# Performance work log

Hardware: AMD Instinct MI355X
Metric: run time of the kernel (lower is better)

The kernel has to match this reference:

```python
import jax, jax.numpy as jnp
import numpy as np

NUM_HEADS = 16  # matches init_kwargs num_heads
ROPE_BASE = 10000.0


def _rope(x):
    # x: [B, H, T, d_k]; canonical interleaved rotary embedding
    d = x.shape[-1]
    T = x.shape[-2]
    inv_freq = 1.0 / (ROPE_BASE ** (jnp.arange(0, d, 2, dtype=jnp.float32) / d))  # [d/2]
    ang = jnp.arange(T, dtype=jnp.float32)[:, None] * inv_freq[None, :]  # [T, d/2]
    cos, sin = jnp.cos(ang), jnp.sin(ang)  # broadcast over B,H
    x1 = x[..., 0::2]
    x2 = x[..., 1::2]
    even = x1 * cos - x2 * sin
    odd = x1 * sin + x2 * cos
    return jnp.stack([even, odd], axis=-1).reshape(x.shape)


def setup_inputs() -> dict:
    key = jax.random.key(0)
    ks = jax.random.split(key, 5)
    B, T, D = 2, 2048, 2048
    s = 1.0 / np.sqrt(D)
    return {
        "x": jax.random.normal(ks[0], (B, T, D), dtype=jnp.float32),
        "Wkqv": jax.random.normal(ks[1], (D, 3 * D), dtype=jnp.float32) * s,
        "bkqv": jax.random.normal(ks[2], (3 * D,), dtype=jnp.float32) * 0.01,
        "Wo": jax.random.normal(ks[3], (D, D), dtype=jnp.float32) * s,
        "bo": jax.random.normal(ks[4], (D,), dtype=jnp.float32) * 0.01,
    }


def reference(x, Wkqv, bkqv, Wo, bo):
    B, T, D = x.shape
    H = NUM_HEADS
    d_k = D // H
    kqv = x @ Wkqv + bkqv  # [B, T, 3D]
    # split order per source: index 0 = K, 1 = Q, 2 = V
    k, q, v = jnp.split(kqv, 3, axis=-1)

    def heads(t):  # [B, T, D] -> [B, H, T, d_k]
        return t.reshape(B, T, H, d_k).transpose(0, 2, 1, 3)

    k, q, v = heads(k), heads(q), heads(v)
    k = _rope(k)
    q = _rope(q)
    scores = jnp.einsum('bhtd,bhTd->bhtT', q, k)  # [B, H, T, T]
    causal = jnp.triu(jnp.ones((T, T), dtype=bool), k=1)
    scores = jnp.where(causal, -jnp.inf, scores)
    attn = jax.nn.softmax(scores / jnp.sqrt(jnp.float32(d_k)), axis=-1)
    out = jnp.einsum('bhtT,bhTd->bhtd', attn, v)  # [B, H, T, d_k]
    out = out.transpose(0, 2, 1, 3).reshape(B, T, D)
    return out @ Wo + bo
```

## Files before the change

### kernel.cpp

```cpp
#include <hip/hip_runtime.h>
#include <cstdint>
#include <cstddef>

typedef __attribute__((ext_vector_type(4))) float  floatx4;
typedef __attribute__((ext_vector_type(8))) __bf16 bf16x8;
typedef __attribute__((ext_vector_type(4))) __bf16 bf16x4;

#define B_   2
#define T_   2048
#define D_   2048
#define H_   16
#define DK   128
#define BT_  (B_ * T_)
#define N3   (3 * D_)

__device__ __forceinline__ void async_copy16(const void* g, void* l) {
    __builtin_amdgcn_global_load_lds((const __attribute__((address_space(1))) void*)g,
                                     (__attribute__((address_space(3))) void*)l,
                                     16, 0, 0);
}

__global__ void cast_bf16_kernel(const float* __restrict__ in, __bf16* __restrict__ out, int n4) {
    int i = blockIdx.x * 256 + threadIdx.x;
    if (i >= n4) return;
    float4 v = ((const float4*)in)[i];
    bf16x4 o;
    o.x = (__bf16)v.x; o.y = (__bf16)v.y; o.z = (__bf16)v.z; o.w = (__bf16)v.w;
    ((bf16x4*)out)[i] = o;
}

__global__ __launch_bounds__(256)
void transcast_kernel(const float* __restrict__ in, __bf16* __restrict__ out, int R, int C) {
    __shared__ float tile[64][65];
    const int tid = threadIdx.x;
    const int r0 = blockIdx.y * 64, c0 = blockIdx.x * 64;
#pragma unroll
    for (int p = 0; p < 4; ++p) {
        int u = p * 256 + tid;
        int r = u >> 4, c4 = (u & 15) * 4;
        float4 v = *(const float4*)(in + (size_t)(r0 + r) * C + c0 + c4);
        tile[r][c4 + 0] = v.x; tile[r][c4 + 1] = v.y;
        tile[r][c4 + 2] = v.z; tile[r][c4 + 3] = v.w;
    }
    __syncthreads();
#pragma unroll
    for (int p = 0; p < 2; ++p) {
        int v = p * 256 + tid;
        int cc = v >> 3, rr = (v & 7) * 8;
        bf16x8 o;
#pragma unroll
        for (int i2 = 0; i2 < 8; ++i2) o[i2] = (__bf16)tile[rr + i2][cc];
        *(bf16x8*)(out + (size_t)(c0 + cc) * R + r0 + rr) = o;
    }
}

template <typename OutT>
__global__ __launch_bounds__(256)
void gemm_bt(const __bf16* __restrict__ A, const __bf16* __restrict__ BTm,
             const float* __restrict__ bias, OutT* __restrict__ C,
             int M, int N, int K) {
    __shared__ __align__(16) __bf16 As[128 * 64];
    __shared__ __align__(16) __bf16 Bs[128 * 64];
    const int tid  = threadIdx.x;
    const int lane = tid & 63;
    const int wave = tid >> 6;
    const int quad = lane >> 4;
    const int l16  = lane & 15;
    const int m0 = blockIdx.y * 128;
    const int n0 = blockIdx.x * 128;
    const int wm = (wave & 1) * 64;
    const int wn = (wave >> 1) * 64;

    const floatx4 z4 = {0.f, 0.f, 0.f, 0.f};
    floatx4 acc[4][4];
#pragma unroll
    for (int i = 0; i < 4; ++i)
#pragma unroll
        for (int j = 0; j < 4; ++j) acc[i][j] = z4;

    int           sOff[4];
    const __bf16* gA[4];
    const __bf16* gB[4];
#pragma unroll
    for (int i = 0; i < 4; ++i) {
        int s = i * 256 + tid;
        int row = s >> 3, cs = s & 7;
        int gc = cs ^ (row & 7);
        sOff[i] = s * 8;
        gA[i] = A   + (size_t)(m0 + row) * K + gc * 8;
        gB[i] = BTm + (size_t)(n0 + row) * K + gc * 8;
    }

    for (int kt = 0; kt < K; kt += 64) {
        __syncthreads();
#pragma unroll
        for (int i = 0; i < 4; ++i) {
            async_copy16(gA[i] + kt, As + sOff[i]);
            async_copy16(gB[i] + kt, Bs + sOff[i]);
        }
        __syncthreads();
#pragma unroll
        for (int ks2 = 0; ks2 < 2; ++ks2) {
            bf16x8 af[4], bf[4];
#pragma unroll
            for (int t = 0; t < 4; ++t) {
                int rowA = wm + t * 16 + l16;
                int ca = (ks2 * 4 + quad) ^ (rowA & 7);
                af[t] = *(const bf16x8*)(As + rowA * 64 + ca * 8);
                int rowB = wn + t * 16 + l16;
                int cb = (ks2 * 4 + quad) ^ (rowB & 7);
                bf[t] = *(const bf16x8*)(Bs + rowB * 64 + cb * 8);
            }
#pragma unroll
            for (int mt = 0; mt < 4; ++mt)
#pragma unroll
                for (int nt = 0; nt < 4; ++nt)
                    acc[mt][nt] = __builtin_amdgcn_mfma_f32_16x16x32_bf16(af[mt], bf[nt], acc[mt][nt], 0, 0, 0);
        }
    }

#pragma unroll
    for (int nt = 0; nt < 4; ++nt) {
        int n = n0 + wn + nt * 16 + l16;
        float bv = bias[n];
#pragma unroll
        for (int mt = 0; mt < 4; ++mt)
#pragma unroll
            for (int r = 0; r < 4; ++r) {
                int m = m0 + wm + mt * 16 + quad * 4 + r;
                C[(size_t)m * N + n] = (OutT)(acc[mt][nt][r] + bv);
            }
    }
}

__global__ __launch_bounds__(256)
void gemm_kqv(const __bf16* __restrict__ A, const __bf16* __restrict__ BTm,
              const float* __restrict__ bias,
              __bf16* __restrict__ Kh, __bf16* __restrict__ Qh,
              __bf16* __restrict__ VT,
              int M, int N, int K) {
    __shared__ __align__(16) __bf16 smem[128 * 136];
    __bf16* As = smem;
    __bf16* Bs = smem + 128 * 64;
    const int tid  = threadIdx.x;
    const int lane = tid & 63;
    const int wave = tid >> 6;
    const int quad = lane >> 4;
    const int l16  = lane & 15;
    const int m0 = blockIdx.y * 128;
    const int n0 = blockIdx.x * 128;
    const int wm = (wave & 1) * 64;
    const int wn = (wave >> 1) * 64;

    const floatx4 z4 = {0.f, 0.f, 0.f, 0.f};
    floatx4 acc[4][4];
#pragma unroll
    for (int i = 0; i < 4; ++i)
#pragma unroll
        for (int j = 0; j < 4; ++j) acc[i][j] = z4;

    int           sOff[4];
    const __bf16* gA[4];
    const __bf16* gB[4];
#pragma unroll
    for (int i = 0; i < 4; ++i) {
        int s = i * 256 + tid;
        int row = s >> 3, cs = s & 7;
        int gc = cs ^ (row & 7);
        sOff[i] = s * 8;
        gA[i] = A   + (size_t)(m0 + row) * K + gc * 8;
        gB[i] = BTm + (size_t)(n0 + row) * K + gc * 8;
    }

    for (int kt = 0; kt < K; kt += 64) {
        __syncthreads();
#pragma unroll
        for (int i = 0; i < 4; ++i) {
            async_copy16(gA[i] + kt, As + sOff[i]);
            async_copy16(gB[i] + kt, Bs + sOff[i]);
        }
        __syncthreads();
#pragma unroll
        for (int ks2 = 0; ks2 < 2; ++ks2) {
            bf16x8 af[4], bf[4];
#pragma unroll
            for (int t = 0; t < 4; ++t) {
                int rowA = wm + t * 16 + l16;
                int ca = (ks2 * 4 + quad) ^ (rowA & 7);
                af[t] = *(const bf16x8*)(As + rowA * 64 + ca * 8);
                int rowB = wn + t * 16 + l16;
                int cb = (ks2 * 4 + quad) ^ (rowB & 7);
                bf[t] = *(const bf16x8*)(Bs + rowB * 64 + cb * 8);
            }
#pragma unroll
            for (int mt = 0; mt < 4; ++mt)
#pragma unroll
                for (int nt = 0; nt < 4; ++nt)
                    acc[mt][nt] = __builtin_amdgcn_mfma_f32_16x16x32_bf16(af[mt], bf[nt], acc[mt][nt], 0, 0, 0);
        }
    }

    const int which = n0 >> 11;
    const int h  = (n0 & (D_ - 1)) >> 7;
    const int b  = m0 >> 11;
    const int t0 = m0 & (T_ - 1);
    const int bh = b * H_ + h;

    if (which == 2) {
        __syncthreads();
#pragma unroll
        for (int nt = 0; nt < 4; ++nt) {
            const int n  = n0 + wn + nt * 16 + l16;
            const float bv = bias[n];
            const int dd = wn + nt * 16 + l16;
#pragma unroll
            for (int mt = 0; mt < 4; ++mt)
#pragma unroll
                for (int r = 0; r < 4; ++r) {
                    const int tl = wm + mt * 16 + quad * 4 + r;
                    smem[dd * 136 + tl] = (__bf16)(acc[mt][nt][r] + bv);
                }
        }
        __syncthreads();
#pragma unroll
        for (int i = 0; i < 8; ++i) {
            int s = i * 256 + tid;
            int dd = s >> 4, c = s & 15;
            bf16x8 vv = *(const bf16x8*)(smem + dd * 136 + c * 8);
            *(bf16x8*)(VT + ((size_t)bh * DK + dd) * T_ + t0 + c * 8) = vv;
        }
    } else {
        const float qscale = which ? 0.12751740f : 1.0f;
        __bf16* dst = which ? Qh : Kh;
#pragma unroll
        for (int nt = 0; nt < 4; ++nt) {
            const int n  = n0 + wn + nt * 16 + l16;
            const float bv = bias[n];
            const int dd = wn + nt * 16 + l16;
            const float freq_rev = 0.15915494309189535f *
                exp2f((float)(dd >> 1) * (-13.287712379549449f / 64.f));
#pragma unroll
            for (int mt = 0; mt < 4; ++mt)
#pragma unroll
                for (int r = 0; r < 4; ++r) {
                    const int t = t0 + wm + mt * 16 + quad * 4 + r;
                    const float val = acc[mt][nt][r] + bv;
                    const float other = __shfl_xor(val, 1);
                    const float x1 = (dd & 1) ? other : val;
                    const float x2 = (dd & 1) ? val : other;
                    float rev = (float)t * freq_rev;
                    rev -= floorf(rev);
                    const float ang = rev * 6.283185307179586f;
                    const float sn = __sinf(ang), cn = __cosf(ang);
                    const float res = (dd & 1) ? (x1 * sn + x2 * cn)
                                               : (x1 * cn - x2 * sn);
                    dst[((size_t)bh * T_ + t) * DK + dd] = (__bf16)(res * qscale);
                }
        }
    }
}

__global__ __launch_bounds__(512)
void fa_kernel(const __bf16* __restrict__ Qg, const __bf16* __restrict__ Kg,
               const __bf16* __restrict__ VTg, __bf16* __restrict__ Og) {
    __shared__ __align__(16) __bf16 Ks[2][64 * 128];
    __shared__ __align__(16) __bf16 Vs[2][128 * 64];
    __shared__ __align__(16) __bf16 Ps[8][16 * 64];
    const int tid  = threadIdx.x;
    const int lane = tid & 63, wave = tid >> 6;
    const int quad = lane >> 4, l16 = lane & 15;
    const int bh = blockIdx.y;
    const int j  = blockIdx.x;
    const int b = bh >> 4, h = bh & 15;

    const __bf16* Kb = Kg  + (size_t)bh * T_ * DK;
    const __bf16* Vb = VTg + (size_t)bh * DK * T_;
    __bf16* Psw = Ps[wave];
    const int swzP = (l16 & 7) << 1;

    const floatx4 z4 = {0.f, 0.f, 0.f, 0.f};

    int           sK[2], sV[2];
    const __bf16* gK[2];
    const __bf16* gV[2];
#pragma unroll
    for (int i = 0; i < 2; ++i) {
        int s = i * 512 + tid;
        { int row = s >> 4, cs = s & 15; int gc = cs ^ (row & 7);
          sK[i] = s * 8; gK[i] = Kb + (size_t)row * DK + gc * 8; }
        { int row = s >> 3, cs = s & 7;  int gc = cs ^ (row & 7);
          sV[i] = s * 8; gV[i] = Vb + (size_t)row * T_ + gc * 8; }
    }

    for (int half = 0; half < 2; ++half) {
        const int qt = half ? (15 - j) : j;
        const int q0 = qt * 128;
        const int qpos = q0 + wave * 16 + l16;
        const int nkt = 2 * qt + 2;

        __syncthreads();
        {
            const __bf16* Qb = Qg + (size_t)(bh * T_ + q0) * DK;
#pragma unroll
            for (int i = 0; i < 4; ++i) {
                int s = i * 512 + tid;
                int row = s >> 4, cs = s & 15;
                int gc = cs ^ (row & 7);
                async_copy16(Qb + row * DK + gc * 8, &Ks[0][0] + s * 8);
            }
        }
        __syncthreads();
        bf16x8 qf[4];
#pragma unroll
        for (int ks = 0; ks < 4; ++ks) {
            int row = wave * 16 + l16;
            int c = (ks * 4 + quad) ^ (row & 7);
            qf[ks] = *(const bf16x8*)(&Ks[0][0] + row * DK + c * 8);
        }
        __syncthreads();

#pragma unroll
        for (int i = 0; i < 2; ++i) async_copy16(gK[i], &Ks[0][0] + sK[i]);
#pragma unroll
        for (int i = 0; i < 2; ++i) async_copy16(gV[i], &Vs[0][0] + sV[i]);

        float m_i = -1e30f, l_i = 0.f;
        floatx4 accO[8];
#pragma unroll
        for (int dt = 0; dt < 8; ++dt) accO[dt] = z4;

        for (int kt = 0; kt < nkt; ++kt) {
            const int cur = kt & 1;
            if (kt < nkt - 1) {
                const int nb = cur ^ 1;
                const size_t koff = (size_t)(kt + 1) * 64 * DK;
                const size_t voff = (size_t)(kt + 1) * 64;
#pragma unroll
                for (int i = 0; i < 2; ++i) async_copy16(gK[i] + koff, &Ks[nb][0] + sK[i]);
#pragma unroll
                for (int i = 0; i < 2; ++i) async_copy16(gV[i] + voff, &Vs[nb][0] + sV[i]);
                asm volatile("s_waitcnt vmcnt(4)" ::: "memory");
            } else {
                asm volatile("s_waitcnt vmcnt(0)" ::: "memory");
            }
            __builtin_amdgcn_s_barrier();

            const __bf16* Kcur = &Ks[cur][0];
            const __bf16* Vcur = &Vs[cur][0];

            floatx4 sc[4];
#pragma unroll
            for (int nt = 0; nt < 4; ++nt) sc[nt] = z4;
            __builtin_amdgcn_s_setprio(1);
#pragma unroll
            for (int ks = 0; ks < 4; ++ks)
#pragma unroll
                for (int nt = 0; nt < 4; ++nt) {
                    int row = nt * 16 + l16;
                    int c = (ks * 4 + quad) ^ (row & 7);
                    bf16x8 kf = *(const bf16x8*)(Kcur + row * DK + c * 8);
                    sc[nt] = __builtin_amdgcn_mfma_f32_16x16x32_bf16(kf, qf[ks], sc[nt], 0, 0, 0);
                }
            __builtin_amdgcn_s_setprio(0);

            float mnew = -1e30f;
            if (kt >= 2 * qt) {
#pragma unroll
                for (int nt = 0; nt < 4; ++nt) {
                    int kbase = kt * 64 + nt * 16 + quad * 4;
#pragma unroll
                    for (int r = 0; r < 4; ++r) {
                        float v = sc[nt][r];
                        v = (kbase + r > qpos) ? -1e30f : v;
                        sc[nt][r] = v;
                        mnew = fmaxf(mnew, v);
                    }
                }
            } else {
#pragma unroll
                for (int nt = 0; nt < 4; ++nt)
#pragma unroll
                    for (int r = 0; r < 4; ++r) mnew = fmaxf(mnew, sc[nt][r]);
            }
            mnew = fmaxf(mnew, __shfl_xor(mnew, 16));
            mnew = fmaxf(mnew, __shfl_xor(mnew, 32));
            const float mi = fmaxf(m_i, mnew);
            const float alpha = exp2f(m_i - mi);
            m_i = mi;

            float rs = 0.f;
#pragma unroll
            for (int nt = 0; nt < 4; ++nt)
#pragma unroll
                for (int r = 0; r < 4; ++r) {
                    float pv = exp2f(sc[nt][r] - mi);
                    sc[nt][r] = pv;
                    rs += pv;
                }
            rs += __shfl_xor(rs, 16);
            rs += __shfl_xor(rs, 32);
            l_i = l_i * alpha + rs;
#pragma unroll
            for (int dt = 0; dt < 8; ++dt)
#pragma unroll
                for (int r = 0; r < 4; ++r) accO[dt][r] *= alpha;

#pragma unroll
            for (int nt = 0; nt < 4; ++nt) {
                bf16x4 pw;
                pw.x = (__bf16)sc[nt][0]; pw.y = (__bf16)sc[nt][1];
                pw.z = (__bf16)sc[nt][2]; pw.w = (__bf16)sc[nt][3];
                int g = (nt * 4 + quad) ^ swzP;
                *(bf16x4*)(Psw + l16 * 64 + g * 4) = pw;
            }
            __builtin_amdgcn_s_setprio(1);
#pragma unroll
            for (int kc = 0; kc < 2; ++kc) {
                int gk = (kc * 8 + quad * 2) ^ swzP;
                bf16x8 pb = *(const bf16x8*)(Psw + l16 * 64 + gk * 4);
#pragma unroll
                for (int dt = 0; dt < 8; ++dt) {
                    int vrow = dt * 16 + l16;
                    int vch = (kc * 4 + quad) ^ (vrow & 7);
                    bf16x8 vf = *(const bf16x8*)(Vcur + vrow * 64 + vch * 8);
                    accO[dt] = __builtin_amdgcn_mfma_f32_16x16x32_bf16(vf, pb, accO[dt], 0, 0, 0);
                }
            }
            __builtin_amdgcn_s_setprio(0);

            __builtin_amdgcn_s_barrier();
        }

        const float inv = 1.0f / l_i;
        __bf16* orow = Og + (size_t)(b * T_ + qpos) * D_ + h * DK;
#pragma unroll
        for (int dt = 0; dt < 8; ++dt) {
            bf16x4 ow;
            ow.x = (__bf16)(accO[dt][0] * inv);
            ow.y = (__bf16)(accO[dt][1] * inv);
            ow.z = (__bf16)(accO[dt][2] * inv);
            ow.w = (__bf16)(accO[dt][3] * inv);
            *(bf16x4*)(orow + dt * 16 + quad * 4) = ow;
        }
    }
}

extern "C" void kernel_launch(void* const* d_in, const int* in_sizes, int n_in,
                              void* d_out, int out_size, void* d_ws, size_t ws_size,
                              hipStream_t stream) {
    const float* x    = (const float*)d_in[0];
    const float* Wkqv = (const float*)d_in[1];
    const float* bkqv = (const float*)d_in[2];
    const float* Wo   = (const float*)d_in[3];
    const float* bo   = (const float*)d_in[4];
    float* out = (float*)d_out;

    char* p = (char*)d_ws;
    __bf16* xb    = (__bf16*)p; p += (size_t)BT_ * D_ * 2;
    __bf16* WkqvT = (__bf16*)p; p += (size_t)D_ * N3 * 2;
    __bf16* WoT   = (__bf16*)p; p += (size_t)D_ * D_ * 2;
    __bf16* qh    = (__bf16*)p; p += (size_t)BT_ * D_ * 2;
    __bf16* kh    = (__bf16*)p; p += (size_t)BT_ * D_ * 2;
    __bf16* vT    = (__bf16*)p; p += (size_t)BT_ * D_ * 2;
    __bf16* ao    = (__bf16*)p; p += (size_t)BT_ * D_ * 2;

    cast_bf16_kernel<<<(BT_ * D_ / 4 + 255) / 256, 256, 0, stream>>>(x, xb, BT_ * D_ / 4);
    transcast_kernel<<<dim3(N3 / 64, D_ / 64), 256, 0, stream>>>(Wkqv, WkqvT, D_, N3);
    transcast_kernel<<<dim3(D_ / 64, D_ / 64), 256, 0, stream>>>(Wo, WoT, D_, D_);
    gemm_kqv<<<dim3(N3 / 128, BT_ / 128), 256, 0, stream>>>(xb, WkqvT, bkqv, kh, qh, vT, BT_, N3, D_);
    fa_kernel<<<dim3(8, B_ * H_), 512, 0, stream>>>(qh, kh, vT, ao);
    gemm_bt<float><<<dim3(D_ / 128, BT_ / 128), 256, 0, stream>>>(ao, WoT, bo, out, BT_, D_, D_);
}
```

Baseline: 402.2 us.

## Deepen attention K/V prefetch, add lazy softmax rescale, swizzle GEMM blocks

The flash-attention kernel moves from a two-slot to a four-slot K/V buffer ring and prefetches two tiles ahead. The per-tile waitcnt is adjusted to match, and the trailing barrier at the end of each iteration is removed, since the slot being overwritten was last read two iterations earlier. The online softmax now rescales the accumulator and running sum only when the row max grows by more than 8 (log2 units), which skips most alpha multiplies at the cost of a wave vote and slightly larger intermediate exponentials. Both GEMM kernels remap the linear block index with a stride-8 swizzle so that consecutive blocks on the same XCD share A/B tiles in cache. The four-slot ring doubles the K/V shared memory, which may reduce occupancy.

```diff
diff --git a/kernel.cpp b/kernel.cpp
--- a/kernel.cpp
+++ b/kernel.cpp
@@ -66,8 +66,11 @@
     const int wave = tid >> 6;
     const int quad = lane >> 4;
     const int l16  = lane & 15;
-    const int m0 = blockIdx.y * 128;
-    const int n0 = blockIdx.x * 128;
+    const int nwg = gridDim.x * gridDim.y;
+    const int lin = blockIdx.y * gridDim.x + blockIdx.x;
+    const int swz = (lin & 7) * (nwg >> 3) + (lin >> 3);
+    const int m0 = (swz / gridDim.x) * 128;
+    const int n0 = (swz % gridDim.x) * 128;
     const int wm = (wave & 1) * 64;
     const int wn = (wave >> 1) * 64;
 
@@ -147,8 +150,11 @@
     const int wave = tid >> 6;
     const int quad = lane >> 4;
     const int l16  = lane & 15;
-    const int m0 = blockIdx.y * 128;
-    const int n0 = blockIdx.x * 128;
+    const int nwg = gridDim.x * gridDim.y;
+    const int lin = blockIdx.y * gridDim.x + blockIdx.x;
+    const int swz = (lin & 7) * (nwg >> 3) + (lin >> 3);
+    const int m0 = (swz / gridDim.x) * 128;
+    const int n0 = (swz % gridDim.x) * 128;
     const int wm = (wave & 1) * 64;
     const int wn = (wave >> 1) * 64;
 
@@ -263,8 +269,8 @@
 __global__ __launch_bounds__(512)
 void fa_kernel(const __bf16* __restrict__ Qg, const __bf16* __restrict__ Kg,
                const __bf16* __restrict__ VTg, __bf16* __restrict__ Og) {
-    __shared__ __align__(16) __bf16 Ks[2][64 * 128];
-    __shared__ __align__(16) __bf16 Vs[2][128 * 64];
+    __shared__ __align__(16) __bf16 Ks[4][64 * 128];
+    __shared__ __align__(16) __bf16 Vs[4][128 * 64];
     __shared__ __align__(16) __bf16 Ps[8][16 * 64];
     const int tid  = threadIdx.x;
     const int lane = tid & 63, wave = tid >> 6;
@@ -320,9 +326,14 @@
         __syncthreads();
 
 #pragma unroll
-        for (int i = 0; i < 2; ++i) async_copy16(gK[i], &Ks[0][0] + sK[i]);
-#pragma unroll
-        for (int i = 0; i < 2; ++i) async_copy16(gV[i], &Vs[0][0] + sV[i]);
+        for (int tl = 0; tl < 2; ++tl) {
+            const size_t koff = (size_t)tl * 64 * DK;
+            const size_t voff = (size_t)tl * 64;
+#pragma unroll
+            for (int i = 0; i < 2; ++i) async_copy16(gK[i] + koff, &Ks[tl][0] + sK[i]);
+#pragma unroll
+            for (int i = 0; i < 2; ++i) async_copy16(gV[i] + voff, &Vs[tl][0] + sV[i]);
+        }
 
         float m_i = -1e30f, l_i = 0.f;
         floatx4 accO[8];
@@ -330,21 +341,22 @@
         for (int dt = 0; dt < 8; ++dt) accO[dt] = z4;
 
         for (int kt = 0; kt < nkt; ++kt) {
-            const int cur = kt & 1;
-            if (kt < nkt - 1) {
-                const int nb = cur ^ 1;
-                const size_t koff = (size_t)(kt + 1) * 64 * DK;
-                const size_t voff = (size_t)(kt + 1) * 64;
-#pragma unroll
-                for (int i = 0; i < 2; ++i) async_copy16(gK[i] + koff, &Ks[nb][0] + sK[i]);
-#pragma unroll
-                for (int i = 0; i < 2; ++i) async_copy16(gV[i] + voff, &Vs[nb][0] + sV[i]);
-                asm volatile("s_waitcnt vmcnt(4)" ::: "memory");
-            } else {
-                asm volatile("s_waitcnt vmcnt(0)" ::: "memory");
-            }
+            if (kt + 2 < nkt) {
+                const int sl = (kt + 2) & 3;
+                const size_t koff = (size_t)(kt + 2) * 64 * DK;
+                const size_t voff = (size_t)(kt + 2) * 64;
+#pragma unroll
+                for (int i = 0; i < 2; ++i) async_copy16(gK[i] + koff, &Ks[sl][0] + sK[i]);
+#pragma unroll
+                for (int i = 0; i < 2; ++i) async_copy16(gV[i] + voff, &Vs[sl][0] + sV[i]);
+            }
+            const int rem = nkt - 1 - kt;
+            if (rem >= 2)      asm volatile("s_waitcnt vmcnt(8)" ::: "memory");
+            else if (rem == 1) asm volatile("s_waitcnt vmcnt(4)" ::: "memory");
+            else               asm volatile("s_waitcnt vmcnt(0)" ::: "memory");
             __builtin_amdgcn_s_barrier();
 
+            const int cur = kt & 3;
             const __bf16* Kcur = &Ks[cur][0];
             const __bf16* Vcur = &Vs[cur][0];
 
@@ -384,26 +396,29 @@
             }
             mnew = fmaxf(mnew, __shfl_xor(mnew, 16));
             mnew = fmaxf(mnew, __shfl_xor(mnew, 32));
-            const float mi = fmaxf(m_i, mnew);
-            const float alpha = exp2f(m_i - mi);
-            m_i = mi;
+            if (!__all(mnew - m_i <= 8.0f)) {
+                const float mi = fmaxf(m_i, mnew);
+                const float alpha = exp2f(m_i - mi);
+                m_i = mi;
+                l_i *= alpha;
+#pragma unroll
+                for (int dt = 0; dt < 8; ++dt)
+#pragma unroll
+                    for (int r = 0; r < 4; ++r) accO[dt][r] *= alpha;
+            }
 
             float rs = 0.f;
 #pragma unroll
             for (int nt = 0; nt < 4; ++nt)
 #pragma unroll
                 for (int r = 0; r < 4; ++r) {
-                    float pv = exp2f(sc[nt][r] - mi);
+                    float pv = exp2f(sc[nt][r] - m_i);
                     sc[nt][r] = pv;
                     rs += pv;
                 }
             rs += __shfl_xor(rs, 16);
             rs += __shfl_xor(rs, 32);
-            l_i = l_i * alpha + rs;
-#pragma unroll
-            for (int dt = 0; dt < 8; ++dt)
-#pragma unroll
-                for (int r = 0; r < 4; ++r) accO[dt][r] *= alpha;
+            l_i += rs;
 
 #pragma unroll
             for (int nt = 0; nt < 4; ++nt) {
@@ -427,8 +442,6 @@
                 }
             }
             __builtin_amdgcn_s_setprio(0);
-
-            __builtin_amdgcn_s_barrier();
         }
 
         const float inv = 1.0f / l_i;
```

Measured after the change: 391.0 us. 1.03x faster.
